# Performance work log

Measured on AMD Instinct MI355X. Metric: run time of the kernel, lower is better.

## Reference

```python
import jax, jax.numpy as jnp
import numpy as np

DIM = 768
N_HEADS = 8
HEAD_DIM = DIM // N_HEADS  # 96
B, T = 4, 2048


def rotate_half(x):
    x1, x2 = jnp.split(x, 2, axis=-1)
    return jnp.concatenate([-x2, x1], axis=-1)


def rope_pos(seq_len, head_dim, dtype=jnp.float32):
    inv_freq = 1.0 / (10000.0 ** (jnp.arange(0, head_dim, 2, dtype=jnp.float32) / head_dim))
    t = jnp.arange(seq_len, dtype=jnp.float32)
    freqs = t[:, None] * inv_freq[None, :]          # [T, head_dim/2]
    return jnp.concatenate([freqs, freqs], axis=-1).astype(dtype)  # [T, head_dim]


def setup_inputs() -> dict:
    key = jax.random.key(0)
    k1, k2, k3, k4, k5 = jax.random.split(key, 5)
    x = jax.random.normal(k1, (B, T, DIM), dtype=jnp.float32)
    # additive causal mask [T, T]: 0 on/below diagonal, -inf above
    neg = jnp.finfo(jnp.float32).min
    mask = jnp.where(jnp.tril(jnp.ones((T, T), dtype=bool)), 0.0, neg).astype(jnp.float32)
    # torch nn.Linear params (y = x @ W.T + b), default-ish init scale
    s_qkv = 1.0 / np.sqrt(DIM)
    w_qkv = jax.random.uniform(k2, (3 * DIM, DIM), minval=-s_qkv, maxval=s_qkv, dtype=jnp.float32)
    b_qkv = jax.random.uniform(k3, (3 * DIM,), minval=-s_qkv, maxval=s_qkv, dtype=jnp.float32)
    w_proj = jax.random.uniform(k4, (DIM, DIM), minval=-s_qkv, maxval=s_qkv, dtype=jnp.float32)
    b_proj = jax.random.uniform(k5, (DIM,), minval=-s_qkv, maxval=s_qkv, dtype=jnp.float32)
    return {"x": x, "mask": mask, "w_qkv": w_qkv, "b_qkv": b_qkv,
            "w_proj": w_proj, "b_proj": b_proj}


def reference(x, mask, w_qkv, b_qkv, w_proj, b_proj):
    Bx, Tx, C = x.shape
    qkv = x @ w_qkv.T + b_qkv                        # [B, T, 3*C]
    qkv = qkv.reshape(Bx, Tx, 3, N_HEADS, HEAD_DIM)
    q, k, v = qkv[:, :, 0], qkv[:, :, 1], qkv[:, :, 2]  # [B, T, H, Dh]
    q = q.transpose(0, 2, 1, 3)                      # [B, H, T, Dh]
    k = k.transpose(0, 2, 1, 3)
    v = v.transpose(0, 2, 1, 3)
    pos = rope_pos(Tx, HEAD_DIM, x.dtype)            # [T, Dh]
    cos_p = jnp.cos(pos)[None, None]
    sin_p = jnp.sin(pos)[None, None]
    q = q * cos_p + rotate_half(q) * sin_p
    k = k * cos_p + rotate_half(k) * sin_p
    scale = 1.0 / np.sqrt(HEAD_DIM)
    scores = jnp.einsum('bhqd,bhkd->bhqk', q, k) * scale
    scores = scores + mask[None, None]               # additive 2D mask
    probs = jax.nn.softmax(scores.astype(jnp.float32), axis=-1).astype(x.dtype)
    out = jnp.einsum('bhqk,bhkd->bhqd', probs, v)    # [B, H, T, Dh]
    out = out.transpose(0, 2, 1, 3).reshape(Bx, Tx, C)
    return out @ w_proj.T + b_proj
```

## Files before the change

kernel.cpp:

```cpp
#include <hip/hip_runtime.h>
#include <hip/hip_bf16.h>

#define DIMC 768
#define NH 8
#define HD 96
#define BB 4
#define TT 2048
#define MTOT (BB*TT)
#define NQKV (3*DIMC)

typedef short bfx8 __attribute__((ext_vector_type(8)));
typedef short sx4  __attribute__((ext_vector_type(4)));
typedef float fx4  __attribute__((ext_vector_type(4)));

__device__ __forceinline__ short f2b(float f) {
    __hip_bfloat16 h = __float2bfloat16(f);
    return __builtin_bit_cast(short, h);
}
__device__ __forceinline__ float b2f(short s) {
    __hip_bfloat16 h = __builtin_bit_cast(__hip_bfloat16, s);
    return __bfloat162float(h);
}

__global__ __launch_bounds__(256) void f2b_kernel(const float* __restrict__ in,
                                                  short* __restrict__ out, int n) {
    int idx = (blockIdx.x * 256 + threadIdx.x) * 8;
    if (idx >= n) return;
    fx4 v0 = *(const fx4*)(in + idx);
    fx4 v1 = *(const fx4*)(in + idx + 4);
    bfx8 r;
    #pragma unroll
    for (int j = 0; j < 4; j++) { r[j] = f2b(v0[j]); r[4 + j] = f2b(v1[j]); }
    *(bfx8*)(out + idx) = r;
}

__global__ __launch_bounds__(256) void rope_table(float* __restrict__ ct, float* __restrict__ st) {
    int idx = blockIdx.x * 256 + threadIdx.x;
    if (idx >= TT * 48) return;
    int t = idx / 48, d = idx - (idx / 48) * 48;
    float f = powf(10000.0f, -(float)(2 * d) / 96.0f);
    float a = (float)t * f;
    ct[idx] = cosf(a);
    st[idx] = sinf(a);
}

__global__ __launch_bounds__(256) void rope_apply(short* __restrict__ q, short* __restrict__ k,
                                                  const float* __restrict__ ct,
                                                  const float* __restrict__ st) {
    int idx = blockIdx.x * 256 + threadIdx.x;
    if (idx >= BB * NH * TT * 48) return;
    int r = idx / 48, d = idx - r * 48;
    int t = r & (TT - 1);
    const float qs = 0.1020620726f;
    float c = ct[t * 48 + d], s = st[t * 48 + d];
    short* qp = q + (size_t)r * HD;
    float x1 = b2f(qp[d]), x2 = b2f(qp[d + 48]);
    qp[d]      = f2b((x1 * c - x2 * s) * qs);
    qp[d + 48] = f2b((x2 * c + x1 * s) * qs);
    short* kp = k + (size_t)r * HD;
    x1 = b2f(kp[d]); x2 = b2f(kp[d + 48]);
    kp[d]      = f2b(x1 * c - x2 * s);
    kp[d + 48] = f2b(x2 * c + x1 * s);
}

template<int EPI>
__global__ __launch_bounds__(256) void gemm_bt(const short* __restrict__ A,
                                               const short* __restrict__ Bw,
                                               const float* __restrict__ bias,
                                               float* __restrict__ outf,
                                               short* __restrict__ qd, short* __restrict__ kd,
                                               short* __restrict__ vt,
                                               int N, int K) {
    __shared__ __align__(16) short Asm[64][40];
    __shared__ __align__(16) short Bsm[64][40];
    __shared__ __align__(16) char  ep[4][32 * 40 * 4];

    int m0 = blockIdx.x * 64;
    int n0 = blockIdx.y * 64;
    int tid = threadIdx.x;
    int w = tid >> 6, lane = tid & 63;
    int wm = w & 1, wn = w >> 1;
    int fr = lane & 15, fq = lane >> 4;
    int srow = tid >> 2, scol = (tid & 3) * 8;

    const short* aptr = A + (size_t)(m0 + srow) * K + scol;
    const short* bptr = Bw + (size_t)(n0 + srow) * K + scol;

    fx4 acc[2][2] = {};
    for (int k0 = 0; k0 < K; k0 += 32) {
        bfx8 av = *(const bfx8*)(aptr + k0);
        bfx8 bv = *(const bfx8*)(bptr + k0);
        *(bfx8*)&Asm[srow][scol] = av;
        *(bfx8*)&Bsm[srow][scol] = bv;
        __syncthreads();
        bfx8 a0 = *(const bfx8*)&Asm[wm * 32 + fr][fq * 8];
        bfx8 a1 = *(const bfx8*)&Asm[wm * 32 + 16 + fr][fq * 8];
        bfx8 b0 = *(const bfx8*)&Bsm[wn * 32 + fr][fq * 8];
        bfx8 b1 = *(const bfx8*)&Bsm[wn * 32 + 16 + fr][fq * 8];
        acc[0][0] = __builtin_amdgcn_mfma_f32_16x16x32_bf16(a0, b0, acc[0][0], 0, 0, 0);
        acc[0][1] = __builtin_amdgcn_mfma_f32_16x16x32_bf16(a0, b1, acc[0][1], 0, 0, 0);
        acc[1][0] = __builtin_amdgcn_mfma_f32_16x16x32_bf16(a1, b0, acc[1][0], 0, 0, 0);
        acc[1][1] = __builtin_amdgcn_mfma_f32_16x16x32_bf16(a1, b1, acc[1][1], 0, 0, 0);
        __syncthreads();
    }

    if (EPI == 0) {
        float (*epf)[32][40] = (float (*)[32][40])ep;
        #pragma unroll
        for (int mt = 0; mt < 2; mt++)
            #pragma unroll
            for (int nt = 0; nt < 2; nt++)
                #pragma unroll
                for (int r = 0; r < 4; r++) {
                    int t = mt * 16 + fq * 4 + r, n = nt * 16 + fr;
                    epf[w][t][n] = acc[mt][nt][r] + bias[n0 + wn * 32 + n];
                }
        __syncthreads();
        int r2 = lane & 31, h2 = lane >> 5;
        int mg = m0 + wm * 32 + r2, ng = n0 + wn * 32 + h2 * 16;
        const float* src = &epf[w][r2][h2 * 16];
        float* dst = outf + (size_t)mg * N + ng;
        #pragma unroll
        for (int j = 0; j < 4; j++) ((fx4*)dst)[j] = ((const fx4*)src)[j];
    } else {
        int part = n0 / DIMC;
        int nrel0 = n0 - part * DIMC + wn * 32;
        if (part < 2) {
            short (*eps)[32][40] = (short (*)[32][40])ep;
            #pragma unroll
            for (int mt = 0; mt < 2; mt++)
                #pragma unroll
                for (int nt = 0; nt < 2; nt++)
                    #pragma unroll
                    for (int r = 0; r < 4; r++) {
                        int t = mt * 16 + fq * 4 + r, n = nt * 16 + fr;
                        eps[w][t][n] = f2b(acc[mt][nt][r] + bias[n0 + wn * 32 + n]);
                    }
            __syncthreads();
            int r2 = lane & 31, h2 = lane >> 5;
            int tg = m0 + wm * 32 + r2;
            int b = tg >> 11, t = tg & (TT - 1);
            int ncol = nrel0 + h2 * 16;
            int hh = ncol / HD, d0 = ncol - hh * HD;
            short* dstp = (part == 0 ? qd : kd) + (((size_t)(b * NH + hh) * TT + t) * HD + d0);
            const short* srcp = &eps[w][r2][h2 * 16];
            ((bfx8*)dstp)[0] = ((const bfx8*)srcp)[0];
            ((bfx8*)dstp)[1] = ((const bfx8*)srcp)[1];
        } else {
            short (*eps)[32][40] = (short (*)[32][40])ep;
            #pragma unroll
            for (int nt = 0; nt < 2; nt++)
                #pragma unroll
                for (int mt = 0; mt < 2; mt++) {
                    sx4 tmp;
                    #pragma unroll
                    for (int r = 0; r < 4; r++)
                        tmp[r] = f2b(acc[mt][nt][r] + bias[n0 + wn * 32 + nt * 16 + fr]);
                    int n = nt * 16 + fr, t0l = mt * 16 + fq * 4;
                    *(sx4*)&eps[w][n][t0l] = tmp;
                }
            __syncthreads();
            int nr = lane & 31, h2 = lane >> 5;
            int dg = nrel0 + nr;
            int hh = dg / HD, d = dg - hh * HD;
            int tg0 = m0 + wm * 32 + h2 * 16;
            int b = tg0 >> 11, t = tg0 & (TT - 1);
            short* dstp = vt + (((size_t)(b * NH + hh) * HD + d) * TT + t);
            const short* srcp = &eps[w][nr][h2 * 16];
            ((bfx8*)dstp)[0] = ((const bfx8*)srcp)[0];
            ((bfx8*)dstp)[1] = ((const bfx8*)srcp)[1];
        }
    }
}

__global__ __launch_bounds__(256, 2) void attn_kernel(const short* __restrict__ Qw,
                                                      const short* __restrict__ Kw,
                                                      const short* __restrict__ VTw,
                                                      short* __restrict__ att) {
    int id = blockIdx.x;
    int xcd = id & 7, j = id >> 3;
    int bh = xcd + 8 * (j & 3);
    int spair = j >> 2;
    int tid = threadIdx.x, w = tid >> 6, lane = tid & 63;
    int fr = lane & 15, fq = lane >> 4;
    const short* Q  = Qw  + (size_t)bh * TT * HD;
    const short* Kp = Kw  + (size_t)bh * TT * HD;
    const short* VT = VTw + (size_t)bh * HD * TT;

    __shared__ __align__(16) short p_lds[4][16][40];
    __shared__ __align__(16) short ep_o[4][16][104];

    int half = w >> 1, wsub = w & 1;
    int subtile = half ? (63 - spair) : spair;
    int qrow = subtile * 32 + wsub * 16;
    const int kend = qrow + 16;

    bfx8 qf[3];
    #pragma unroll
    for (int s = 0; s < 3; s++)
        qf[s] = *(const bfx8*)(Q + (size_t)(qrow + fr) * HD + s * 32 + fq * 8);

    bfx8 ones;
    #pragma unroll
    for (int j2 = 0; j2 < 8; j2++) ones[j2] = (short)0x3F80;

    fx4 o[7] = {};

    bfx8 kf[2][3];
    #pragma unroll
    for (int nt = 0; nt < 2; nt++)
        #pragma unroll
        for (int st = 0; st < 3; st++)
            kf[nt][st] = *(const bfx8*)(Kp + (size_t)(nt * 16 + fr) * HD + st * 32 + fq * 8);

    for (int kk0 = 0; kk0 < kend; kk0 += 32) {
        bfx8 vb[6];
        #pragma unroll
        for (int dt = 0; dt < 6; dt++)
            vb[dt] = *(const bfx8*)(VT + (size_t)(dt * 16 + fr) * TT + kk0 + fq * 8);

        fx4 s2[2] = {};
        #pragma unroll
        for (int nt = 0; nt < 2; nt++)
            #pragma unroll
            for (int st = 0; st < 3; st++)
                s2[nt] = __builtin_amdgcn_mfma_f32_16x16x32_bf16(qf[st], kf[nt][st], s2[nt], 0, 0, 0);

        #pragma unroll
        for (int nt = 0; nt < 2; nt++) {
            int row = kk0 + 32 + nt * 16 + fr;
            row = row < TT ? row : TT - 1;
            #pragma unroll
            for (int st = 0; st < 3; st++)
                kf[nt][st] = *(const bfx8*)(Kp + (size_t)row * HD + st * 32 + fq * 8);
        }

        #pragma unroll
        for (int nt = 0; nt < 2; nt++)
            #pragma unroll
            for (int r = 0; r < 4; r++) {
                int key = kk0 + nt * 16 + fr;
                int qr  = qrow + fq * 4 + r;
                float v = (key > qr) ? -1e30f : s2[nt][r];
                p_lds[w][fq * 4 + r][nt * 16 + fr] = f2b(__expf(v));
            }

        bfx8 pa = *(const bfx8*)&p_lds[w][fr][fq * 8];
        #pragma unroll
        for (int dt = 0; dt < 6; dt++)
            o[dt] = __builtin_amdgcn_mfma_f32_16x16x32_bf16(pa, vb[dt], o[dt], 0, 0, 0);
        o[6] = __builtin_amdgcn_mfma_f32_16x16x32_bf16(pa, ones, o[6], 0, 0, 0);
    }

    float inv[4];
    #pragma unroll
    for (int r = 0; r < 4; r++) inv[r] = 1.f / o[6][r];

    #pragma unroll
    for (int dt = 0; dt < 6; dt++)
        #pragma unroll
        for (int r = 0; r < 4; r++)
            ep_o[w][fq * 4 + r][dt * 16 + fr] = f2b(o[dt][r] * inv[r]);
    int row = lane & 15, seg = lane >> 4;
    int tg = qrow + row;
    int b = bh >> 3, hh = bh & 7;
    short* dst = att + ((size_t)(b * TT + tg)) * DIMC + hh * HD + seg * 24;
    const short* src = &ep_o[w][row][seg * 24];
    #pragma unroll
    for (int j2 = 0; j2 < 3; j2++) ((bfx8*)dst)[j2] = ((const bfx8*)src)[j2];
}

extern "C" void kernel_launch(void* const* d_in, const int* in_sizes, int n_in,
                              void* d_out, int out_size, void* d_ws, size_t ws_size,
                              hipStream_t stream) {
    const float* x     = (const float*)d_in[0];
    const float* wqkv  = (const float*)d_in[2];
    const float* bqkv  = (const float*)d_in[3];
    const float* wproj = (const float*)d_in[4];
    const float* bproj = (const float*)d_in[5];
    float* out = (float*)d_out;

    char* p = (char*)d_ws;
    short* xb     = (short*)p; p += (size_t)MTOT * DIMC * 2;
    short* wqkvb  = (short*)p; p += (size_t)NQKV * DIMC * 2;
    short* wprojb = (short*)p; p += (size_t)DIMC * DIMC * 2;
    short* qws    = (short*)p; p += (size_t)BB * NH * TT * HD * 2;
    short* kws    = (short*)p; p += (size_t)BB * NH * TT * HD * 2;
    short* vtws   = (short*)p; p += (size_t)BB * NH * TT * HD * 2;
    short* attws  = (short*)p; p += (size_t)MTOT * DIMC * 2;
    float* ct     = (float*)p; p += (size_t)TT * 48 * 4;
    float* st     = (float*)p; p += (size_t)TT * 48 * 4;

    f2b_kernel<<<(MTOT * DIMC / 8 + 255) / 256, 256, 0, stream>>>(x, xb, MTOT * DIMC);
    f2b_kernel<<<(NQKV * DIMC / 8 + 255) / 256, 256, 0, stream>>>(wqkv, wqkvb, NQKV * DIMC);
    f2b_kernel<<<(DIMC * DIMC / 8 + 255) / 256, 256, 0, stream>>>(wproj, wprojb, DIMC * DIMC);
    rope_table<<<(TT * 48 + 255) / 256, 256, 0, stream>>>(ct, st);

    dim3 g1(MTOT / 64, NQKV / 64);
    gemm_bt<1><<<g1, 256, 0, stream>>>(xb, wqkvb, bqkv, nullptr, qws, kws, vtws, NQKV, DIMC);

    rope_apply<<<(BB * NH * TT * 48 + 255) / 256, 256, 0, stream>>>(qws, kws, ct, st);

    attn_kernel<<<1024, 256, 0, stream>>>(qws, kws, vtws, attws);

    dim3 g3(MTOT / 64, DIMC / 64);
    gemm_bt<0><<<g3, 256, 0, stream>>>(attws, wprojb, bproj, out, nullptr, nullptr, nullptr, DIMC, DIMC);
}
```

Before: 349.7 us.

## Split attention key loop across two wave slices and reduce partial outputs in LDS

Doubles the attention block to 512 threads so that two groups of four waves each handle alternating 32-key chunks of the same query rows. Slice 1 writes its fp32 partial output and row sums to shared memory, and slice 0 combines them, normalizes and writes bf16 results directly to global memory. The aim is more parallelism and better latency hiding along the serial key loop. The cost is more LDS, an extra block-wide barrier, and a scalar-strided global store in place of the earlier vectorized store. The block-to-(batch, head) mapping also changes, which drops the previous XCD-aware interleave.

```diff
diff --git a/kernel.cpp b/kernel.cpp
--- a/kernel.cpp
+++ b/kernel.cpp
@@ -173,24 +173,23 @@
     }
 }
 
-__global__ __launch_bounds__(256, 2) void attn_kernel(const short* __restrict__ Qw,
+__global__ __launch_bounds__(512, 8) void attn_kernel(const short* __restrict__ Qw,
                                                       const short* __restrict__ Kw,
                                                       const short* __restrict__ VTw,
                                                       short* __restrict__ att) {
     int id = blockIdx.x;
-    int xcd = id & 7, j = id >> 3;
-    int bh = xcd + 8 * (j & 3);
-    int spair = j >> 2;
+    int bh = id & 31, spair = id >> 5;
     int tid = threadIdx.x, w = tid >> 6, lane = tid & 63;
+    int w4 = w & 3, slice = w >> 2;
     int fr = lane & 15, fq = lane >> 4;
     const short* Q  = Qw  + (size_t)bh * TT * HD;
     const short* Kp = Kw  + (size_t)bh * TT * HD;
     const short* VT = VTw + (size_t)bh * HD * TT;
 
-    __shared__ __align__(16) short p_lds[4][16][40];
-    __shared__ __align__(16) short ep_o[4][16][104];
-
-    int half = w >> 1, wsub = w & 1;
+    __shared__ __align__(16) short p_lds[8][16][40];
+    __shared__ __align__(16) float pf[4][16][100];
+
+    int half = w4 >> 1, wsub = w4 & 1;
     int subtile = half ? (63 - spair) : spair;
     int qrow = subtile * 32 + wsub * 16;
     const int kend = qrow + 16;
@@ -206,14 +205,15 @@
 
     fx4 o[7] = {};
 
+    int kk_start = slice * 32;
     bfx8 kf[2][3];
     #pragma unroll
     for (int nt = 0; nt < 2; nt++)
         #pragma unroll
         for (int st = 0; st < 3; st++)
-            kf[nt][st] = *(const bfx8*)(Kp + (size_t)(nt * 16 + fr) * HD + st * 32 + fq * 8);
-
-    for (int kk0 = 0; kk0 < kend; kk0 += 32) {
+            kf[nt][st] = *(const bfx8*)(Kp + (size_t)(kk_start + nt * 16 + fr) * HD + st * 32 + fq * 8);
+
+    for (int kk0 = kk_start; kk0 < kend; kk0 += 64) {
         bfx8 vb[6];
         #pragma unroll
         for (int dt = 0; dt < 6; dt++)
@@ -228,7 +228,7 @@
 
         #pragma unroll
         for (int nt = 0; nt < 2; nt++) {
-            int row = kk0 + 32 + nt * 16 + fr;
+            int row = kk0 + 64 + nt * 16 + fr;
             row = row < TT ? row : TT - 1;
             #pragma unroll
             for (int st = 0; st < 3; st++)
@@ -252,22 +252,31 @@
         o[6] = __builtin_amdgcn_mfma_f32_16x16x32_bf16(pa, ones, o[6], 0, 0, 0);
     }
 
-    float inv[4];
-    #pragma unroll
-    for (int r = 0; r < 4; r++) inv[r] = 1.f / o[6][r];
-
-    #pragma unroll
-    for (int dt = 0; dt < 6; dt++)
-        #pragma unroll
-        for (int r = 0; r < 4; r++)
-            ep_o[w][fq * 4 + r][dt * 16 + fr] = f2b(o[dt][r] * inv[r]);
-    int row = lane & 15, seg = lane >> 4;
-    int tg = qrow + row;
-    int b = bh >> 3, hh = bh & 7;
-    short* dst = att + ((size_t)(b * TT + tg)) * DIMC + hh * HD + seg * 24;
-    const short* src = &ep_o[w][row][seg * 24];
-    #pragma unroll
-    for (int j2 = 0; j2 < 3; j2++) ((bfx8*)dst)[j2] = ((const bfx8*)src)[j2];
+    if (slice == 1) {
+        #pragma unroll
+        for (int dt = 0; dt < 6; dt++)
+            #pragma unroll
+            for (int r = 0; r < 4; r++)
+                pf[w4][fq * 4 + r][dt * 16 + fr] = o[dt][r];
+        if (fr == 0) {
+            #pragma unroll
+            for (int r = 0; r < 4; r++) pf[w4][fq * 4 + r][96] = o[6][r];
+        }
+    }
+    __syncthreads();
+    if (slice == 0) {
+        int b = bh >> 3, hh = bh & 7;
+        #pragma unroll
+        for (int r = 0; r < 4; r++) {
+            int i = fq * 4 + r;
+            float inv = 1.f / (o[6][r] + pf[w4][i][96]);
+            int tg = qrow + i;
+            short* dst = att + ((size_t)(b * TT + tg)) * DIMC + hh * HD + fr;
+            #pragma unroll
+            for (int dt = 0; dt < 6; dt++)
+                dst[dt * 16] = f2b((o[dt][r] + pf[w4][i][dt * 16 + fr]) * inv);
+        }
+    }
 }
 
 extern "C" void kernel_launch(void* const* d_in, const int* in_sizes, int n_in,
@@ -301,7 +310,7 @@
 
     rope_apply<<<(BB * NH * TT * 48 + 255) / 256, 256, 0, stream>>>(qws, kws, ct, st);
 
-    attn_kernel<<<1024, 256, 0, stream>>>(qws, kws, vtws, attws);
+    attn_kernel<<<1024, 512, 0, stream>>>(qws, kws, vtws, attws);
 
     dim3 g3(MTOT / 64, DIMC / 64);
     gemm_bt<0><<<g3, 256, 0, stream>>>(attws, wprojb, bproj, out, nullptr, nullptr, nullptr, DIMC, DIMC);
```

New measurement: 441.8 us. +26.3%, slower.
